# Kernel tuning notes

Hardware: AMD Instinct MI355X
Metric: run time of the kernel (lower is better)

## Reference

```python
import jax, jax.numpy as jnp
import numpy as np

N_NODES = 100000

def setup_inputs() -> dict:
    key = jax.random.key(0)
    k1, k2, k3, k4 = jax.random.split(key, 4)
    nfeat, nhid = 128, 128
    features = jax.random.normal(k1, (N_NODES, nfeat), dtype=jnp.float32)
    edges = jax.random.randint(k2, (2, 1600000), 0, N_NODES, dtype=jnp.int64)
    # Linear(nfeature, nhidden) params (PyTorch layout: W [out, in], b [out])
    bound = 1.0 / np.sqrt(nfeat)
    W = jax.random.uniform(k3, (nhid, nfeat), dtype=jnp.float32, minval=-bound, maxval=bound)
    b = jax.random.uniform(k4, (nhid,), dtype=jnp.float32, minval=-bound, maxval=bound)
    return {"features": features, "edges": edges, "W": W, "b": b}

def reference(features, edges, W, b):
    n = features.shape[0]
    # add self loops
    loops = jnp.arange(n, dtype=edges.dtype)
    row = jnp.concatenate([edges[0], loops])  # source
    col = jnp.concatenate([edges[1], loops])  # target
    # linear transform
    x = features @ W.T + b  # [N, nhid]
    # degree over source indices (PyG message uses degree(row, size[0]))
    deg = jax.ops.segment_sum(jnp.ones_like(row, dtype=x.dtype), row, num_segments=n)
    dis = jax.lax.rsqrt(deg)  # deg >= 1 thanks to self loops
    norm = dis[row] * dis[col]  # [E']
    msgs = norm[:, None] * x[row]  # gather + scale, [E', nhid]
    out = jax.ops.segment_sum(msgs, col, num_segments=n)  # scatter-add to targets
    return out
```

## Files before the change

kernel.cpp:

```cpp
#include <hip/hip_runtime.h>

#define NFEAT 128
#define CH 25600
#define CH2 (CH / 2)

__launch_bounds__(256)
__global__ void hist16_kernel(const int* __restrict__ rows, const int* __restrict__ cols,
                              unsigned int* __restrict__ ph_row, unsigned int* __restrict__ ph_col,
                              int* __restrict__ rank, int E, int n, int W, int log_epb) {
    __shared__ unsigned int h[CH2];
    const int b = blockIdx.x;
    const int c0 = blockIdx.y * CH;
    const int z = blockIdx.z;
    const int* __restrict__ keys = z ? cols : rows;
    unsigned int* __restrict__ ph = z ? ph_col : ph_row;

    for (int i = threadIdx.x; i < CH2; i += 256) h[i] = 0;
    __syncthreads();

    const int lo = b << log_epb;
    const int hi = min(E, lo + (1 << log_epb));
    const int t = threadIdx.x;

    int full = (hi - lo) >> 10;
    for (int it = 0; it < full; ++it) {
        int e0 = lo + (it << 10) + t * 4;
        int4 kk = *(const int4*)(keys + e0);
        int k0 = kk.x - c0, k1 = kk.y - c0, k2 = kk.z - c0, k3 = kk.w - c0;
        if ((unsigned)k0 < CH) {
            unsigned old = atomicAdd(&h[k0 >> 1], 1u << ((k0 & 1) * 16));
            if (z) rank[e0 + 0] = (old >> ((k0 & 1) * 16)) & 0xffff;
        }
        if ((unsigned)k1 < CH) {
            unsigned old = atomicAdd(&h[k1 >> 1], 1u << ((k1 & 1) * 16));
            if (z) rank[e0 + 1] = (old >> ((k1 & 1) * 16)) & 0xffff;
        }
        if ((unsigned)k2 < CH) {
            unsigned old = atomicAdd(&h[k2 >> 1], 1u << ((k2 & 1) * 16));
            if (z) rank[e0 + 2] = (old >> ((k2 & 1) * 16)) & 0xffff;
        }
        if ((unsigned)k3 < CH) {
            unsigned old = atomicAdd(&h[k3 >> 1], 1u << ((k3 & 1) * 16));
            if (z) rank[e0 + 3] = (old >> ((k3 & 1) * 16)) & 0xffff;
        }
    }
    for (int e = lo + (full << 10) + t; e < hi; e += 256) {
        int k = keys[e] - c0;
        if ((unsigned)k < CH) {
            unsigned old = atomicAdd(&h[k >> 1], 1u << ((k & 1) * 16));
            if (z) rank[e] = (old >> ((k & 1) * 16)) & 0xffff;
        }
    }
    __syncthreads();

    int wbase = c0 >> 1;
    for (int i = threadIdx.x; i < CH2; i += 256) {
        int w = wbase + i;
        if (w < W) ph[(size_t)b * W + w] = h[i];
    }
}

__global__ void cum_kernel(const unsigned short* __restrict__ ph_row,
                           unsigned short* __restrict__ ph_col,
                           float* __restrict__ dis, int* __restrict__ colcnt, int NB, int n) {
    int k = blockIdx.x * 256 + threadIdx.x;
    if (k >= n) return;
    int rs = 0;
    for (int b = 0; b < NB; ++b) rs += ph_row[(size_t)b * n + k];
    dis[k] = rsqrtf(1.0f + (float)rs);
    int acc = 0;
    for (int b = 0; b < NB; ++b) {
        int v = ph_col[(size_t)b * n + k];
        ph_col[(size_t)b * n + k] = (unsigned short)acc;
        acc += v;
    }
    colcnt[k] = acc;
}

__global__ void scan_bsum_kernel(const int* __restrict__ cnt, int* __restrict__ bsum, int n) {
    __shared__ int s[256];
    int base = blockIdx.x * 1024;
    int t = threadIdx.x;
    int v = 0;
#pragma unroll
    for (int i = 0; i < 4; ++i) {
        int idx = base + t * 4 + i;
        if (idx < n) v += cnt[idx];
    }
    s[t] = v;
    __syncthreads();
    for (int o = 128; o > 0; o >>= 1) {
        if (t < o) s[t] += s[t + o];
        __syncthreads();
    }
    if (t == 0) bsum[blockIdx.x] = s[0];
}

__global__ void scan_top_kernel(int* __restrict__ bsum, int nb) {
    __shared__ int s[256];
    int t = threadIdx.x;
    int v = (t < nb) ? bsum[t] : 0;
    s[t] = v;
    __syncthreads();
    for (int o = 1; o < 256; o <<= 1) {
        int add = (t >= o) ? s[t - o] : 0;
        __syncthreads();
        s[t] += add;
        __syncthreads();
    }
    if (t < nb) bsum[t] = s[t] - v;
}

__global__ void scan_write_kernel(const int* __restrict__ cnt, const int* __restrict__ bsum,
                                  int* __restrict__ off, int n) {
    __shared__ int s[256];
    int base = blockIdx.x * 1024;
    int t = threadIdx.x;
    int v[4];
    int sum = 0;
#pragma unroll
    for (int i = 0; i < 4; ++i) {
        int idx = base + t * 4 + i;
        v[i] = (idx < n) ? cnt[idx] : 0;
        sum += v[i];
    }
    s[t] = sum;
    __syncthreads();
    for (int o = 1; o < 256; o <<= 1) {
        int add = (t >= o) ? s[t - o] : 0;
        __syncthreads();
        s[t] += add;
        __syncthreads();
    }
    int p = bsum[blockIdx.x] + s[t] - sum;
#pragma unroll
    for (int i = 0; i < 4; ++i) {
        int idx = base + t * 4 + i;
        if (idx < n) { off[idx] = p; p += v[i]; }
    }
}

__global__ void scatter2_kernel(const int* __restrict__ rows, const int* __restrict__ cols,
                                const int* __restrict__ rank, const unsigned short* __restrict__ ph_col,
                                const int* __restrict__ off, int* __restrict__ rows_buf,
                                int E, int n, int log_epb) {
    int base = blockIdx.x * 1024 + threadIdx.x;
#pragma unroll
    for (int u = 0; u < 4; ++u) {
        int e = base + u * 256;
        if (e < E) {
            int k = cols[e];
            int b = e >> log_epb;
            int pos = off[k] + (int)ph_col[(size_t)b * n + k] + rank[e];
            rows_buf[pos] = rows[e];
        }
    }
}

__launch_bounds__(256, 3)
__global__ void gemm_kernel(const float* __restrict__ feat, const float* __restrict__ W,
                            const float* __restrict__ b, float* __restrict__ x, int n) {
    __shared__ float WT[64][128];
    __shared__ float F[32][68];

    const int t = threadIdx.x;
    const int row0 = blockIdx.x * 32;
    const int c0 = (t & 31) * 4;
    const int r0 = (t >> 5) * 4;

    float4 bb = *(const float4*)(b + c0);
    float4 acc0 = bb, acc1 = bb, acc2 = bb, acc3 = bb;

    for (int kh = 0; kh < 2; ++kh) {
        {
            int c = t >> 1;
            int kb = (t & 1) * 32;
            const float4* src = (const float4*)(W + (size_t)c * NFEAT + kh * 64 + kb);
#pragma unroll
            for (int i = 0; i < 8; ++i) {
                float4 w4 = src[i];
                int k = kb + i * 4;
                WT[k + 0][c] = w4.x;
                WT[k + 1][c] = w4.y;
                WT[k + 2][c] = w4.z;
                WT[k + 3][c] = w4.w;
            }
        }
        {
            int r = t >> 3;
            int kb = (t & 7) * 8;
            int gr = row0 + r;
            float4 a = make_float4(0.f, 0.f, 0.f, 0.f);
            float4 d = a;
            if (gr < n) {
                const float4* src = (const float4*)(feat + (size_t)gr * NFEAT + kh * 64 + kb);
                a = src[0];
                d = src[1];
            }
            *(float4*)&F[r][kb] = a;
            *(float4*)&F[r][kb + 4] = d;
        }
        __syncthreads();

#pragma unroll 2
        for (int k = 0; k < 64; k += 4) {
            float4 w0 = *(const float4*)&WT[k + 0][c0];
            float4 w1 = *(const float4*)&WT[k + 1][c0];
            float4 w2 = *(const float4*)&WT[k + 2][c0];
            float4 w3 = *(const float4*)&WT[k + 3][c0];

            float4 f0 = *(const float4*)&F[r0 + 0][k];
            float4 f1 = *(const float4*)&F[r0 + 1][k];
            float4 f2 = *(const float4*)&F[r0 + 2][k];
            float4 f3 = *(const float4*)&F[r0 + 3][k];

            acc0.x = fmaf(f0.x, w0.x, acc0.x); acc0.y = fmaf(f0.x, w0.y, acc0.y);
            acc0.z = fmaf(f0.x, w0.z, acc0.z); acc0.w = fmaf(f0.x, w0.w, acc0.w);
            acc0.x = fmaf(f0.y, w1.x, acc0.x); acc0.y = fmaf(f0.y, w1.y, acc0.y);
            acc0.z = fmaf(f0.y, w1.z, acc0.z); acc0.w = fmaf(f0.y, w1.w, acc0.w);
            acc0.x = fmaf(f0.z, w2.x, acc0.x); acc0.y = fmaf(f0.z, w2.y, acc0.y);
            acc0.z = fmaf(f0.z, w2.z, acc0.z); acc0.w = fmaf(f0.z, w2.w, acc0.w);
            acc0.x = fmaf(f0.w, w3.x, acc0.x); acc0.y = fmaf(f0.w, w3.y, acc0.y);
            acc0.z = fmaf(f0.w, w3.z, acc0.z); acc0.w = fmaf(f0.w, w3.w, acc0.w);

            acc1.x = fmaf(f1.x, w0.x, acc1.x); acc1.y = fmaf(f1.x, w0.y, acc1.y);
            acc1.z = fmaf(f1.x, w0.z, acc1.z); acc1.w = fmaf(f1.x, w0.w, acc1.w);
            acc1.x = fmaf(f1.y, w1.x, acc1.x); acc1.y = fmaf(f1.y, w1.y, acc1.y);
            acc1.z = fmaf(f1.y, w1.z, acc1.z); acc1.w = fmaf(f1.y, w1.w, acc1.w);
            acc1.x = fmaf(f1.z, w2.x, acc1.x); acc1.y = fmaf(f1.z, w2.y, acc1.y);
            acc1.z = fmaf(f1.z, w2.z, acc1.z); acc1.w = fmaf(f1.z, w2.w, acc1.w);
            acc1.x = fmaf(f1.w, w3.x, acc1.x); acc1.y = fmaf(f1.w, w3.y, acc1.y);
            acc1.z = fmaf(f1.w, w3.z, acc1.z); acc1.w = fmaf(f1.w, w3.w, acc1.w);

            acc2.x = fmaf(f2.x, w0.x, acc2.x); acc2.y = fmaf(f2.x, w0.y, acc2.y);
            acc2.z = fmaf(f2.x, w0.z, acc2.z); acc2.w = fmaf(f2.x, w0.w, acc2.w);
            acc2.x = fmaf(f2.y, w1.x, acc2.x); acc2.y = fmaf(f2.y, w1.y, acc2.y);
            acc2.z = fmaf(f2.y, w1.z, acc2.z); acc2.w = fmaf(f2.y, w1.w, acc2.w);
            acc2.x = fmaf(f2.z, w2.x, acc2.x); acc2.y = fmaf(f2.z, w2.y, acc2.y);
            acc2.z = fmaf(f2.z, w2.z, acc2.z); acc2.w = fmaf(f2.z, w2.w, acc2.w);
            acc2.x = fmaf(f2.w, w3.x, acc2.x); acc2.y = fmaf(f2.w, w3.y, acc2.y);
            acc2.z = fmaf(f2.w, w3.z, acc2.z); acc2.w = fmaf(f2.w, w3.w, acc2.w);

            acc3.x = fmaf(f3.x, w0.x, acc3.x); acc3.y = fmaf(f3.x, w0.y, acc3.y);
            acc3.z = fmaf(f3.x, w0.z, acc3.z); acc3.w = fmaf(f3.x, w0.w, acc3.w);
            acc3.x = fmaf(f3.y, w1.x, acc3.x); acc3.y = fmaf(f3.y, w1.y, acc3.y);
            acc3.z = fmaf(f3.y, w1.z, acc3.z); acc3.w = fmaf(f3.y, w1.w, acc3.w);
            acc3.x = fmaf(f3.z, w2.x, acc3.x); acc3.y = fmaf(f3.z, w2.y, acc3.y);
            acc3.z = fmaf(f3.z, w2.z, acc3.z); acc3.w = fmaf(f3.z, w2.w, acc3.w);
            acc3.x = fmaf(f3.w, w3.x, acc3.x); acc3.y = fmaf(f3.w, w3.y, acc3.y);
            acc3.z = fmaf(f3.w, w3.z, acc3.z); acc3.w = fmaf(f3.w, w3.w, acc3.w);
        }
        __syncthreads();
    }

    int gr = row0 + r0;
    if (gr + 0 < n) *(float4*)(x + (size_t)(gr + 0) * NFEAT + c0) = acc0;
    if (gr + 1 < n) *(float4*)(x + (size_t)(gr + 1) * NFEAT + c0) = acc1;
    if (gr + 2 < n) *(float4*)(x + (size_t)(gr + 2) * NFEAT + c0) = acc2;
    if (gr + 3 < n) *(float4*)(x + (size_t)(gr + 3) * NFEAT + c0) = acc3;
}

__launch_bounds__(256)
__global__ void gather_kernel(const int* __restrict__ rows_buf, const int* __restrict__ off,
                              const int* __restrict__ cnt, const float* __restrict__ x,
                              const float* __restrict__ dis, float* __restrict__ out, int n) {
    int lane = threadIdx.x & 63;
    int c = blockIdx.x * 4 + (threadIdx.x >> 6);
    if (c >= n) return;

    float disc = dis[c];
    int start = off[c];
    int len = cnt[c];
    const float2* x2 = (const float2*)x;

    float2 acc;
    {
        float2 xv = x2[(size_t)c * 64 + lane];
        float sl = disc * disc;
        acc.x = xv.x * sl;
        acc.y = xv.y * sl;
    }

    for (int base = 0; base < len; base += 64) {
        int m = min(64, len - base);
        int r_l = 0;
        float nrm_l = 0.0f;
        if (lane < m) {
            r_l = rows_buf[start + base + lane];
            nrm_l = dis[r_l] * disc;
        }
#pragma unroll 4
        for (int j = 0; j < m; ++j) {
            int r = __shfl(r_l, j);
            float nm = __shfl(nrm_l, j);
            float2 a = x2[(size_t)r * 64 + lane];
            acc.x = fmaf(a.x, nm, acc.x);
            acc.y = fmaf(a.y, nm, acc.y);
        }
    }

    ((float2*)out)[(size_t)c * 64 + lane] = acc;
}

extern "C" void kernel_launch(void* const* d_in, const int* in_sizes, int n_in,
                              void* d_out, int out_size, void* d_ws, size_t ws_size,
                              hipStream_t stream) {
    const float* feat = (const float*)d_in[0];
    const int*   edges = (const int*)d_in[1];
    const float* W = (const float*)d_in[2];
    const float* b = (const float*)d_in[3];
    float* out = (float*)d_out;

    int n = in_sizes[0] / NFEAT;
    int E = in_sizes[1] / 2;
    const int* row = edges;
    const int* col = edges + E;

    int Wd = (n + 1) / 2;
    int nchunk = (n + CH - 1) / CH;

    size_t fixed = (size_t)n * NFEAT + 3 * (size_t)n + 2 * (size_t)E + 256;

    int log_epb = 16;
    int NB = (E + (1 << 16) - 1) >> 16;
    for (int lg = 14; lg <= 16; ++lg) {
        int nb_try = (E + (1 << lg) - 1) >> lg;
        size_t words = fixed + 2 * (size_t)nb_try * Wd;
        if (words * 4 <= ws_size) { log_epb = lg; NB = nb_try; break; }
    }

    float* x        = (float*)d_ws;
    float* dis      = x + (size_t)n * NFEAT;
    int*   colcnt   = (int*)(dis + n);
    int*   off      = colcnt + n;
    int*   rows_buf = off + n;
    int*   rank     = rows_buf + E;
    int*   bsum     = rank + E;
    unsigned int* ph_row = (unsigned int*)(bsum + 256);
    unsigned int* ph_col = ph_row + (size_t)NB * Wd;

    int nb = (n + 1023) / 1024;

    dim3 hgrid(NB, nchunk, 2);
    hist16_kernel<<<hgrid, 256, 0, stream>>>(row, col, ph_row, ph_col, rank, E, n, Wd, log_epb);

    cum_kernel<<<(n + 255) / 256, 256, 0, stream>>>((const unsigned short*)ph_row,
                                                    (unsigned short*)ph_col, dis, colcnt, NB, n);

    scan_bsum_kernel<<<nb, 256, 0, stream>>>(colcnt, bsum, n);
    scan_top_kernel<<<1, 256, 0, stream>>>(bsum, nb);
    scan_write_kernel<<<nb, 256, 0, stream>>>(colcnt, bsum, off, n);

    scatter2_kernel<<<(E + 1023) / 1024, 256, 0, stream>>>(row, col, rank,
                                                           (const unsigned short*)ph_col,
                                                           off, rows_buf, E, n, log_epb);

    gemm_kernel<<<(n + 31) / 32, 256, 0, stream>>>(feat, W, b, x, n);

    gather_kernel<<<(n + 3) / 4, 256, 0, stream>>>(rows_buf, off, colcnt, x, dis, out, n);
}
```

Before: 413.0 us.

## Use split-bf16 MFMA for linear layer and float4 two-edge gather

Replaces the FP32 FMA GEMM with an MFMA kernel that splits both operands into bf16 hi/lo parts and accumulates three products, approximating fp32 accuracy on the matrix cores. Weights are pre-swizzled into LDS in the MFMA operand layout. The gather kernel now has each half-wavefront process alternate edges with float4 loads, then combines the halves with a cross-lane shuffle, so each wave issues wider loads and handles two edges per iteration. The split-bf16 scheme loses a small amount of precision, and the gather adds a reduction step at the end.

Measured after the change: 395.2 us. 4.3% less time.

```diff
diff --git a/kernel.cpp b/kernel.cpp
--- a/kernel.cpp
+++ b/kernel.cpp
@@ -3,6 +3,19 @@
 #define NFEAT 128
 #define CH 25600
 #define CH2 (CH / 2)
+
+typedef __attribute__((ext_vector_type(8))) short bf16x8;
+typedef __attribute__((ext_vector_type(4))) float f32x4;
+
+static __device__ __forceinline__ short f2bf(float f) {
+    unsigned u = __builtin_bit_cast(unsigned, f);
+    unsigned r = (u + 0x7fff + ((u >> 16) & 1)) >> 16;
+    return (short)r;
+}
+static __device__ __forceinline__ float bf2f(short s) {
+    unsigned u = ((unsigned)(unsigned short)s) << 16;
+    return __builtin_bit_cast(float, u);
+}
 
 __launch_bounds__(256)
 __global__ void hist16_kernel(const int* __restrict__ rows, const int* __restrict__ cols,
@@ -157,107 +170,90 @@
     }
 }
 
-__launch_bounds__(256, 3)
-__global__ void gemm_kernel(const float* __restrict__ feat, const float* __restrict__ W,
-                            const float* __restrict__ b, float* __restrict__ x, int n) {
-    __shared__ float WT[64][128];
-    __shared__ float F[32][68];
+__launch_bounds__(256, 2)
+__global__ void gemm_mfma_kernel(const float* __restrict__ feat, const float* __restrict__ W,
+                                 const float* __restrict__ b, float* __restrict__ x, int n) {
+    __shared__ short whi[16384];
+    __shared__ short wlo[16384];
 
     const int t = threadIdx.x;
-    const int row0 = blockIdx.x * 32;
-    const int c0 = (t & 31) * 4;
-    const int r0 = (t >> 5) * 4;
-
-    float4 bb = *(const float4*)(b + c0);
-    float4 acc0 = bb, acc1 = bb, acc2 = bb, acc3 = bb;
-
-    for (int kh = 0; kh < 2; ++kh) {
-        {
-            int c = t >> 1;
-            int kb = (t & 1) * 32;
-            const float4* src = (const float4*)(W + (size_t)c * NFEAT + kh * 64 + kb);
+
+    {
+        int c = t >> 1;
+        int kbase = (t & 1) * 64;
+        int ct = c >> 4;
+        int cl = c & 15;
+#pragma unroll
+        for (int kc = 0; kc < 8; ++kc) {
+            int k0 = kbase + kc * 8;
+            const float4* src = (const float4*)(W + (size_t)c * NFEAT + k0);
+            float4 fa = src[0];
+            float4 fb = src[1];
+            float fv[8] = {fa.x, fa.y, fa.z, fa.w, fb.x, fb.y, fb.z, fb.w};
+            short h8[8], l8[8];
 #pragma unroll
             for (int i = 0; i < 8; ++i) {
-                float4 w4 = src[i];
-                int k = kb + i * 4;
-                WT[k + 0][c] = w4.x;
-                WT[k + 1][c] = w4.y;
-                WT[k + 2][c] = w4.z;
-                WT[k + 3][c] = w4.w;
+                short hi = f2bf(fv[i]);
+                h8[i] = hi;
+                l8[i] = f2bf(fv[i] - bf2f(hi));
             }
-        }
-        {
-            int r = t >> 3;
-            int kb = (t & 7) * 8;
-            int gr = row0 + r;
-            float4 a = make_float4(0.f, 0.f, 0.f, 0.f);
-            float4 d = a;
-            if (gr < n) {
-                const float4* src = (const float4*)(feat + (size_t)gr * NFEAT + kh * 64 + kb);
-                a = src[0];
-                d = src[1];
-            }
-            *(float4*)&F[r][kb] = a;
-            *(float4*)&F[r][kb + 4] = d;
-        }
-        __syncthreads();
-
-#pragma unroll 2
-        for (int k = 0; k < 64; k += 4) {
-            float4 w0 = *(const float4*)&WT[k + 0][c0];
-            float4 w1 = *(const float4*)&WT[k + 1][c0];
-            float4 w2 = *(const float4*)&WT[k + 2][c0];
-            float4 w3 = *(const float4*)&WT[k + 3][c0];
-
-            float4 f0 = *(const float4*)&F[r0 + 0][k];
-            float4 f1 = *(const float4*)&F[r0 + 1][k];
-            float4 f2 = *(const float4*)&F[r0 + 2][k];
-            float4 f3 = *(const float4*)&F[r0 + 3][k];
-
-            acc0.x = fmaf(f0.x, w0.x, acc0.x); acc0.y = fmaf(f0.x, w0.y, acc0.y);
-            acc0.z = fmaf(f0.x, w0.z, acc0.z); acc0.w = fmaf(f0.x, w0.w, acc0.w);
-            acc0.x = fmaf(f0.y, w1.x, acc0.x); acc0.y = fmaf(f0.y, w1.y, acc0.y);
-            acc0.z = fmaf(f0.y, w1.z, acc0.z); acc0.w = fmaf(f0.y, w1.w, acc0.w);
-            acc0.x = fmaf(f0.z, w2.x, acc0.x); acc0.y = fmaf(f0.z, w2.y, acc0.y);
-            acc0.z = fmaf(f0.z, w2.z, acc0.z); acc0.w = fmaf(f0.z, w2.w, acc0.w);
-            acc0.x = fmaf(f0.w, w3.x, acc0.x); acc0.y = fmaf(f0.w, w3.y, acc0.y);
-            acc0.z = fmaf(f0.w, w3.z, acc0.z); acc0.w = fmaf(f0.w, w3.w, acc0.w);
-
-            acc1.x = fmaf(f1.x, w0.x, acc1.x); acc1.y = fmaf(f1.x, w0.y, acc1.y);
-            acc1.z = fmaf(f1.x, w0.z, acc1.z); acc1.w = fmaf(f1.x, w0.w, acc1.w);
-            acc1.x = fmaf(f1.y, w1.x, acc1.x); acc1.y = fmaf(f1.y, w1.y, acc1.y);
-            acc1.z = fmaf(f1.y, w1.z, acc1.z); acc1.w = fmaf(f1.y, w1.w, acc1.w);
-            acc1.x = fmaf(f1.z, w2.x, acc1.x); acc1.y = fmaf(f1.z, w2.y, acc1.y);
-            acc1.z = fmaf(f1.z, w2.z, acc1.z); acc1.w = fmaf(f1.z, w2.w, acc1.w);
-            acc1.x = fmaf(f1.w, w3.x, acc1.x); acc1.y = fmaf(f1.w, w3.y, acc1.y);
-            acc1.z = fmaf(f1.w, w3.z, acc1.z); acc1.w = fmaf(f1.w, w3.w, acc1.w);
-
-            acc2.x = fmaf(f2.x, w0.x, acc2.x); acc2.y = fmaf(f2.x, w0.y, acc2.y);
-            acc2.z = fmaf(f2.x, w0.z, acc2.z); acc2.w = fmaf(f2.x, w0.w, acc2.w);
-            acc2.x = fmaf(f2.y, w1.x, acc2.x); acc2.y = fmaf(f2.y, w1.y, acc2.y);
-            acc2.z = fmaf(f2.y, w1.z, acc2.z); acc2.w = fmaf(f2.y, w1.w, acc2.w);
-            acc2.x = fmaf(f2.z, w2.x, acc2.x); acc2.y = fmaf(f2.z, w2.y, acc2.y);
-            acc2.z = fmaf(f2.z, w2.z, acc2.z); acc2.w = fmaf(f2.z, w2.w, acc2.w);
-            acc2.x = fmaf(f2.w, w3.x, acc2.x); acc2.y = fmaf(f2.w, w3.y, acc2.y);
-            acc2.z = fmaf(f2.w, w3.z, acc2.z); acc2.w = fmaf(f2.w, w3.w, acc2.w);
-
-            acc3.x = fmaf(f3.x, w0.x, acc3.x); acc3.y = fmaf(f3.x, w0.y, acc3.y);
-            acc3.z = fmaf(f3.x, w0.z, acc3.z); acc3.w = fmaf(f3.x, w0.w, acc3.w);
-            acc3.x = fmaf(f3.y, w1.x, acc3.x); acc3.y = fmaf(f3.y, w1.y, acc3.y);
-            acc3.z = fmaf(f3.y, w1.z, acc3.z); acc3.w = fmaf(f3.y, w1.w, acc3.w);
-            acc3.x = fmaf(f3.z, w2.x, acc3.x); acc3.y = fmaf(f3.z, w2.y, acc3.y);
-            acc3.z = fmaf(f3.z, w2.z, acc3.z); acc3.w = fmaf(f3.z, w2.w, acc3.w);
-            acc3.x = fmaf(f3.w, w3.x, acc3.x); acc3.y = fmaf(f3.w, w3.y, acc3.y);
-            acc3.z = fmaf(f3.w, w3.z, acc3.z); acc3.w = fmaf(f3.w, w3.w, acc3.w);
-        }
-        __syncthreads();
-    }
-
-    int gr = row0 + r0;
-    if (gr + 0 < n) *(float4*)(x + (size_t)(gr + 0) * NFEAT + c0) = acc0;
-    if (gr + 1 < n) *(float4*)(x + (size_t)(gr + 1) * NFEAT + c0) = acc1;
-    if (gr + 2 < n) *(float4*)(x + (size_t)(gr + 2) * NFEAT + c0) = acc2;
-    if (gr + 3 < n) *(float4*)(x + (size_t)(gr + 3) * NFEAT + c0) = acc3;
+            int kq = k0 >> 5;
+            int lane = ((k0 & 31) >> 3) * 16 + cl;
+            int idx = ((ct * 4 + kq) * 64 + lane) * 8;
+            *(bf16x8*)&whi[idx] = *(bf16x8*)h8;
+            *(bf16x8*)&wlo[idx] = *(bf16x8*)l8;
+        }
+    }
+    __syncthreads();
+
+    const int lane = t & 63;
+    const int w = t >> 6;
+    const int r0 = blockIdx.x * 64 + w * 16;
+    const int arow = r0 + (lane & 15);
+    const int koff = (lane >> 4) * 8;
+
+    bf16x8 ahi[4], alo[4];
+#pragma unroll
+    for (int kq = 0; kq < 4; ++kq) {
+        float fv[8] = {0, 0, 0, 0, 0, 0, 0, 0};
+        if (arow < n) {
+            const float4* src = (const float4*)(feat + (size_t)arow * NFEAT + kq * 32 + koff);
+            float4 fa = src[0];
+            float4 fb = src[1];
+            fv[0] = fa.x; fv[1] = fa.y; fv[2] = fa.z; fv[3] = fa.w;
+            fv[4] = fb.x; fv[5] = fb.y; fv[6] = fb.z; fv[7] = fb.w;
+        }
+        short h8[8], l8[8];
+#pragma unroll
+        for (int i = 0; i < 8; ++i) {
+            short hi = f2bf(fv[i]);
+            h8[i] = hi;
+            l8[i] = f2bf(fv[i] - bf2f(hi));
+        }
+        ahi[kq] = *(bf16x8*)h8;
+        alo[kq] = *(bf16x8*)l8;
+    }
+
+#pragma unroll
+    for (int ct = 0; ct < 8; ++ct) {
+        f32x4 acc = {0.f, 0.f, 0.f, 0.f};
+#pragma unroll
+        for (int kq = 0; kq < 4; ++kq) {
+            int idx = ((ct * 4 + kq) * 64 + lane) * 8;
+            bf16x8 bh = *(const bf16x8*)&whi[idx];
+            bf16x8 bl = *(const bf16x8*)&wlo[idx];
+            acc = __builtin_amdgcn_mfma_f32_16x16x32_bf16(ahi[kq], bh, acc, 0, 0, 0);
+            acc = __builtin_amdgcn_mfma_f32_16x16x32_bf16(alo[kq], bh, acc, 0, 0, 0);
+            acc = __builtin_amdgcn_mfma_f32_16x16x32_bf16(ahi[kq], bl, acc, 0, 0, 0);
+        }
+        int col = ct * 16 + (lane & 15);
+        float bb = b[col];
+#pragma unroll
+        for (int reg = 0; reg < 4; ++reg) {
+            int row = r0 + (lane >> 4) * 4 + reg;
+            if (row < n) x[(size_t)row * NFEAT + col] = acc[reg] + bb;
+        }
+    }
 }
 
 __launch_bounds__(256)
@@ -265,20 +261,21 @@
                               const int* __restrict__ cnt, const float* __restrict__ x,
                               const float* __restrict__ dis, float* __restrict__ out, int n) {
     int lane = threadIdx.x & 63;
+    int h = lane >> 5;
+    int fl = lane & 31;
     int c = blockIdx.x * 4 + (threadIdx.x >> 6);
     if (c >= n) return;
 
     float disc = dis[c];
     int start = off[c];
     int len = cnt[c];
-    const float2* x2 = (const float2*)x;
-
-    float2 acc;
-    {
-        float2 xv = x2[(size_t)c * 64 + lane];
+    const float4* x4 = (const float4*)x;
+
+    float4 acc = make_float4(0.f, 0.f, 0.f, 0.f);
+    if (h == 0) {
+        float4 xv = x4[(size_t)c * 32 + fl];
         float sl = disc * disc;
-        acc.x = xv.x * sl;
-        acc.y = xv.y * sl;
+        acc.x = xv.x * sl; acc.y = xv.y * sl; acc.z = xv.z * sl; acc.w = xv.w * sl;
     }
 
     for (int base = 0; base < len; base += 64) {
@@ -289,17 +286,26 @@
             r_l = rows_buf[start + base + lane];
             nrm_l = dis[r_l] * disc;
         }
+        int pairs = (m + 1) >> 1;
 #pragma unroll 4
-        for (int j = 0; j < m; ++j) {
-            int r = __shfl(r_l, j);
-            float nm = __shfl(nrm_l, j);
-            float2 a = x2[(size_t)r * 64 + lane];
+        for (int jj = 0; jj < pairs; ++jj) {
+            int src = 2 * jj + h;
+            int r = __shfl(r_l, src);
+            float nm = __shfl(nrm_l, src);
+            float4 a = x4[(size_t)r * 32 + fl];
             acc.x = fmaf(a.x, nm, acc.x);
             acc.y = fmaf(a.y, nm, acc.y);
-        }
-    }
-
-    ((float2*)out)[(size_t)c * 64 + lane] = acc;
+            acc.z = fmaf(a.z, nm, acc.z);
+            acc.w = fmaf(a.w, nm, acc.w);
+        }
+    }
+
+    acc.x += __shfl_xor(acc.x, 32);
+    acc.y += __shfl_xor(acc.y, 32);
+    acc.z += __shfl_xor(acc.z, 32);
+    acc.w += __shfl_xor(acc.w, 32);
+
+    if (h == 0) ((float4*)out)[(size_t)c * 32 + fl] = acc;
 }
 
 extern "C" void kernel_launch(void* const* d_in, const int* in_sizes, int n_in,
@@ -320,7 +326,6 @@
     int nchunk = (n + CH - 1) / CH;
 
     size_t fixed = (size_t)n * NFEAT + 3 * (size_t)n + 2 * (size_t)E + 256;
-
     int log_epb = 16;
     int NB = (E + (1 << 16) - 1) >> 16;
     for (int lg = 14; lg <= 16; ++lg) {
@@ -355,7 +360,7 @@
                                                            (const unsigned short*)ph_col,
                                                            off, rows_buf, E, n, log_epb);
 
-    gemm_kernel<<<(n + 31) / 32, 256, 0, stream>>>(feat, W, b, x, n);
+    gemm_mfma_kernel<<<(n + 63) / 64, 256, 0, stream>>>(feat, W, b, x, n);
 
     gather_kernel<<<(n + 3) / 4, 256, 0, stream>>>(rows_buf, off, colcnt, x, dis, out, n);
 }
```
